# Optimization experiments

Measured on AMD Instinct MI355X. Metric: run time of the kernel, lower is better.

## Reference

```python
import jax, jax.numpy as jnp
import numpy as np

N = 64    # state dim n
K = 8     # mixture components
H = 1024  # fhat hidden
B = 65536
LOG2PI = float(np.log(2.0 * np.pi))

def setup_inputs() -> dict:
    key = jax.random.key(0)
    ks = jax.random.split(key, 8)
    x = jax.random.normal(ks[0], (B, N), jnp.float32)
    y = jax.random.normal(ks[1], (B, 1, N), jnp.float32)
    W1 = jax.random.normal(ks[2], (N, H), jnp.float32) / np.sqrt(N)
    b1 = jnp.zeros((H,), jnp.float32)
    W2 = jax.random.normal(ks[3], (H, 2 * K * N), jnp.float32) / np.sqrt(H)
    b2 = jnp.zeros((2 * K * N,), jnp.float32)
    Wp1 = jax.random.normal(ks[4], (N, N), jnp.float32) / np.sqrt(N)
    bp1 = jnp.zeros((N,), jnp.float32)
    Wp2 = jax.random.normal(ks[5], (N, K), jnp.float32) / np.sqrt(N)
    bp2 = jnp.zeros((K,), jnp.float32)
    return {"x": x, "y": y, "W1": W1, "b1": b1, "W2": W2, "b2": b2,
            "Wp1": Wp1, "bp1": bp1, "Wp2": Wp2, "bp2": bp2}

def _mdn_view(t):
    # torch.stack(t.split(n, dim=1)).view(-1, k, n): raw reshape of [k,B,n] -> [B,k,n]
    return jnp.stack(jnp.split(t, K, axis=1)).reshape(-1, K, N)

def reference(x, y, W1, b1, W2, b2, Wp1, bp1, Wp2, bp2):
    # fhat: Linear -> ELU -> Linear
    fhatx = jax.nn.elu(x @ W1 + b1) @ W2 + b2          # [B, 2*K*N]
    mu_raw, var_raw = jnp.split(fhatx, 2, axis=-1)     # each [B, K*N]
    mu = _mdn_view(mu_raw)                             # [B, K, N]
    var = jnp.maximum(jnp.exp(_mdn_view(var_raw)), 1e-8)
    # pi network: log probs of OneHotCategorical
    logits = jax.nn.elu(x @ Wp1 + bp1) @ Wp2 + bp2     # [B, K]
    log_pi = jax.nn.log_softmax(logits, axis=-1)
    # diagonal-covariance MVN log_prob (closed form, O(n))
    d = y - mu                                         # [B, K, N]
    logp_y = -0.5 * (jnp.sum(d * d / var + jnp.log(var), axis=-1) + N * LOG2PI)
    loss = jax.scipy.special.logsumexp(log_pi + logp_y, axis=-1)  # [B]
    return -jnp.mean(loss)
```

## Files before the change

kernel.cpp:

```cpp
#include <hip/hip_runtime.h>
#include <math.h>

typedef __attribute__((ext_vector_type(8))) _Float16 half8;
typedef __attribute__((ext_vector_type(4))) _Float16 half4;
typedef __attribute__((ext_vector_type(4))) float f32x4;

#define B_TOT 65536
#define LOG2PI_F 1.8378770664093453f
#define HALF_N_LOG2PI (0.5f * 64.0f * LOG2PI_F)
#define LOG_1EM8 (-18.420680743952367f)

#define WS_W2S  0
#define WS_W1P  (2u*1024*1024)
#define WS_LPS  (4u*1024*1024)
#define WS_PART (6u*1024*1024)
#define WS_HP   (8u*1024*1024)

typedef __attribute__((address_space(3))) unsigned int lds_u32;
typedef const __attribute__((address_space(1))) unsigned int glb_u32;

__device__ __forceinline__ void gload16(const void* g, void* l) {
    __builtin_amdgcn_global_load_lds((glb_u32*)g, (lds_u32*)l, 16, 0, 0);
}

__device__ __forceinline__ float eluf(float v) {
    return v > 0.0f ? v : __expf(v) - 1.0f;
}

__global__ __launch_bounds__(256)
void pack_w1(const float* __restrict__ src, _Float16* __restrict__ dst)
{
    __shared__ float ts[64][65];
    const int t = threadIdx.x;
    const int n0 = blockIdx.y * 64;
    {
        int r = t >> 2, c4 = t & 3;
        for (int i = 0; i < 4; ++i) {
            int cc = i * 4 + c4;
            float4 v = *(const float4*)&src[(size_t)r * 1024 + n0 + cc * 4];
            ts[r][cc*4+0] = v.x; ts[r][cc*4+1] = v.y;
            ts[r][cc*4+2] = v.z; ts[r][cc*4+3] = v.w;
        }
    }
    __syncthreads();
    {
        int n = t >> 2;
        for (int i = 0; i < 4; ++i) {
            int k = (i * 4 + (t & 3)) * 4;
            half4 h;
            h.x = (_Float16)ts[k+0][n];
            h.y = (_Float16)ts[k+1][n];
            h.z = (_Float16)ts[k+2][n];
            h.w = (_Float16)ts[k+3][n];
            size_t off = (size_t)(k >> 5) * 32768 + (size_t)(n0 + n) * 32 + (k & 31);
            *(half4*)&dst[off] = h;
        }
    }
}

__global__ __launch_bounds__(256)
void pack_w2s(const float* __restrict__ src, _Float16* __restrict__ dst)
{
    __shared__ float ts[64][65];
    const int t = threadIdx.x;
    const int k0 = blockIdx.x * 64, n0 = blockIdx.y * 64;
    {
        int r = t >> 2, c4 = t & 3;
        for (int i = 0; i < 4; ++i) {
            int cc = i * 4 + c4;
            float4 v = *(const float4*)&src[(size_t)(k0 + r) * 1024 + n0 + cc * 4];
            ts[r][cc*4+0] = v.x; ts[r][cc*4+1] = v.y;
            ts[r][cc*4+2] = v.z; ts[r][cc*4+3] = v.w;
        }
    }
    __syncthreads();
    {
        int n = t >> 2;
        int ng = n0 + n;
        for (int i = 0; i < 4; ++i) {
            int kl = (i * 4 + (t & 3)) * 4;
            int k = k0 + kl;
            half4 h;
            h.x = (_Float16)ts[kl+0][n];
            h.y = (_Float16)ts[kl+1][n];
            h.z = (_Float16)ts[kl+2][n];
            h.w = (_Float16)ts[kl+3][n];
            int kk = k & 31;
            int slot = ((kk >> 3) ^ ((ng >> 1) & 3));
            size_t off = (size_t)(k >> 5) * 32768 + (size_t)ng * 32 + (slot << 3) + (kk & 7);
            *(half4*)&dst[off] = h;
        }
    }
}

__global__ __launch_bounds__(512)
void k1_h(const float* __restrict__ x, const _Float16* __restrict__ W1P,
          const float* __restrict__ b1, _Float16* __restrict__ hp)
{
    __shared__ __align__(16) _Float16 xs[32 * 64];
    __shared__ __align__(16) _Float16 stage[32768];
    const int t = threadIdx.x, q = blockIdx.x;
    const int w = t >> 6, l = t & 63, g = l >> 4, l15 = l & 15;

    {
        const float4* x4 = (const float4*)x;
        int r = t >> 4, c = t & 15;
        float4 v = x4[(size_t)(q * 32 + r) * 16 + c];
        float vv[4] = {v.x, v.y, v.z, v.w};
        #pragma unroll
        for (int i = 0; i < 4; ++i) {
            int col = c * 4 + i;
            xs[r * 64 + (col ^ ((r & 7) << 3))] = (_Float16)vv[i];
        }
    }
    __syncthreads();

    f32x4 acc[8][2];
    const float4* b1_4 = (const float4*)b1;
    #pragma unroll
    for (int nf = 0; nf < 8; ++nf) {
        float4 bv = b1_4[(w * 128 + nf * 16 + 4 * g) >> 2];
        acc[nf][0] = (f32x4){bv.x, bv.y, bv.z, bv.w};
        acc[nf][1] = acc[nf][0];
    }
    #pragma unroll
    for (int k0 = 0; k0 < 64; k0 += 32) {
        half8 bx[2];
        #pragma unroll
        for (int rf = 0; rf < 2; ++rf) {
            int row = rf * 16 + l15;
            bx[rf] = *(const half8*)&xs[row * 64 + ((k0 + 8 * g) ^ ((row & 7) << 3))];
        }
        #pragma unroll
        for (int nf = 0; nf < 8; ++nf) {
            size_t off = (size_t)(k0 >> 5) * 32768 + (size_t)(w * 128 + nf * 16 + l15) * 32 + 8 * g;
            half8 aw = *(const half8*)&W1P[off];
            #pragma unroll
            for (int rf = 0; rf < 2; ++rf)
                acc[nf][rf] = __builtin_amdgcn_mfma_f32_16x16x32_f16(aw, bx[rf], acc[nf][rf], 0, 0, 0);
        }
    }
    #pragma unroll
    for (int nf = 0; nf < 8; ++nf) {
        int kt = w * 4 + (nf >> 1);
        int kkhi = (nf & 1) * 2 + (g >> 1);
        int kklo = 4 * (g & 1);
        #pragma unroll
        for (int rf = 0; rf < 2; ++rf) {
            int row = rf * 16 + l15;
            int slot = kkhi ^ ((row >> 1) & 3);
            half4 h4;
            h4.x = (_Float16)eluf(acc[nf][rf][0]);
            h4.y = (_Float16)eluf(acc[nf][rf][1]);
            h4.z = (_Float16)eluf(acc[nf][rf][2]);
            h4.w = (_Float16)eluf(acc[nf][rf][3]);
            *(half4*)&stage[kt * 1024 + row * 32 + slot * 8 + kklo] = h4;
        }
    }
    __syncthreads();
    #pragma unroll
    for (int i = 0; i < 8; ++i) {
        int f8 = (i * 512 + t) * 8;
        int kt = f8 >> 10;
        int rem = f8 & 1023;
        *(half8*)&hp[(size_t)kt * 2097152 + (size_t)q * 1024 + rem] = *(const half8*)&stage[f8];
    }
}

__global__ __launch_bounds__(512)
void k2_gemm2(const _Float16* __restrict__ hp, const _Float16* __restrict__ W2S,
              const float* __restrict__ b2, const float* __restrict__ y,
              float* __restrict__ lps)
{
    __shared__ __align__(16) _Float16 Ab[2][4096];
    __shared__ __align__(16) _Float16 Bb[2][8192];
    __shared__ float lpp[128][2][2];

    const int t = threadIdx.x;
    const int bid = blockIdx.x;
    const int logical = (bid & 7) * 256 + (bid >> 3);
    const int RT = logical >> 2;
    const int j  = logical & 3;
    const int w = t >> 6, l = t & 63, g = l >> 4, l15 = l & 15;
    const int wr = w >> 2, wc = w & 3;

    int bn[4];
    bn[0] = (wc >> 1) * 64 + (wc & 1) * 32 + l15;
    bn[1] = bn[0] + 16;
    bn[2] = bn[0] + 128;
    bn[3] = bn[1] + 128;

    f32x4 acc[4][4];
    #pragma unroll
    for (int fc = 0; fc < 4; ++fc) {
        int colg = (fc < 2) ? (j * 128 + bn[fc]) : (512 + j * 128 + bn[fc] - 128);
        float bv = b2[colg];
        #pragma unroll
        for (int fr = 0; fr < 4; ++fr) acc[fr][fc] = (f32x4){bv, bv, bv, bv};
    }

    const char* hpb  = (const char*)hp;
    const char* w2sb = (const char*)W2S;
    const int lane16 = l * 16;

    {
        size_t ga = ((size_t)0 * 65536 + (size_t)RT * 128) * 64 + w * 1024 + lane16;
        gload16(hpb + ga, (char*)&Ab[0][0] + w * 1024);
        size_t gb0 = ((size_t)0 * 1024 + j * 128) * 64 + w * 1024 + lane16;
        gload16(w2sb + gb0, (char*)&Bb[0][0] + w * 1024);
        size_t gb1 = ((size_t)0 * 1024 + 512 + j * 128) * 64 + w * 1024 + lane16;
        gload16(w2sb + gb1, (char*)&Bb[0][0] + 8192 + w * 1024);
    }
    __syncthreads();

    for (int kt = 0; kt < 32; ++kt) {
        int cur = kt & 1;
        if (kt < 31) {
            int nx = cur ^ 1;
            size_t ga = ((size_t)(kt + 1) * 65536 + (size_t)RT * 128) * 64 + w * 1024 + lane16;
            gload16(hpb + ga, (char*)&Ab[nx][0] + w * 1024);
            size_t gb0 = ((size_t)(kt + 1) * 1024 + j * 128) * 64 + w * 1024 + lane16;
            gload16(w2sb + gb0, (char*)&Bb[nx][0] + w * 1024);
            size_t gb1 = ((size_t)(kt + 1) * 1024 + 512 + j * 128) * 64 + w * 1024 + lane16;
            gload16(w2sb + gb1, (char*)&Bb[nx][0] + 8192 + w * 1024);
        }
        half8 aF[4], bF[4];
        #pragma unroll
        for (int fr = 0; fr < 4; ++fr) {
            int r = wr * 64 + fr * 16 + l15;
            aF[fr] = *(const half8*)((const char*)&Ab[cur][0] + r * 64 + ((g ^ ((r >> 1) & 3)) << 4));
        }
        #pragma unroll
        for (int fc = 0; fc < 4; ++fc) {
            int n = bn[fc];
            bF[fc] = *(const half8*)((const char*)&Bb[cur][0] + n * 64 + ((g ^ ((n >> 1) & 3)) << 4));
        }
        #pragma unroll
        for (int fc = 0; fc < 4; ++fc)
            #pragma unroll
            for (int fr = 0; fr < 4; ++fr)
                acc[fr][fc] = __builtin_amdgcn_mfma_f32_16x16x32_f16(aF[fr], bF[fc], acc[fr][fc], 0, 0, 0);
        __syncthreads();
    }

    const int jj = j * 2 + (wc >> 1);
    float s[4][4];
    #pragma unroll
    for (int fr = 0; fr < 4; ++fr)
        #pragma unroll
        for (int rg = 0; rg < 4; ++rg) s[fr][rg] = 0.0f;

    #pragma unroll
    for (int fc = 0; fc < 2; ++fc) {
        int n = (wc & 1) * 32 + fc * 16 + l15;
        #pragma unroll
        for (int fr = 0; fr < 4; ++fr)
            #pragma unroll
            for (int rg = 0; rg < 4; ++rg) {
                int grow = RT * 128 + wr * 64 + fr * 16 + 4 * g + rg;
                int bp = (grow >> 3) + jj * 8192;
                float yv = y[(size_t)bp * 64 + n];
                float mu = acc[fr][fc][rg];
                float vr = acc[fr][fc + 2][rg];
                float vre = fmaxf(vr, LOG_1EM8);
                float iv = (vr >= LOG_1EM8) ? expf(-vr) : 1e8f;
                float d = yv - mu;
                s[fr][rg] += fmaf(d * d, iv, vre);
            }
    }
    #pragma unroll
    for (int fr = 0; fr < 4; ++fr)
        #pragma unroll
        for (int rg = 0; rg < 4; ++rg) {
            float v = s[fr][rg];
            v += __shfl_xor(v, 1); v += __shfl_xor(v, 2);
            v += __shfl_xor(v, 4); v += __shfl_xor(v, 8);
            s[fr][rg] = v;
        }
    if (l15 == 0) {
        #pragma unroll
        for (int fr = 0; fr < 4; ++fr)
            #pragma unroll
            for (int rg = 0; rg < 4; ++rg)
                lpp[wr * 64 + fr * 16 + 4 * g + rg][wc >> 1][wc & 1] = s[fr][rg];
    }
    __syncthreads();
    if (t < 256) {
        int row_l = t >> 1, m = t & 1;
        float lp = -0.5f * (lpp[row_l][m][0] + lpp[row_l][m][1]) - HALF_N_LOG2PI;
        int grow = RT * 128 + row_l;
        int bp = (grow >> 3) + (j * 2 + m) * 8192;
        lps[(size_t)bp * 8 + (grow & 7)] = lp;
    }
}

__global__ __launch_bounds__(256)
void k3_pi(const float* __restrict__ x, const float* __restrict__ Wp1,
           const float* __restrict__ bp1, const float* __restrict__ Wp2,
           const float* __restrict__ bp2, const float* __restrict__ lps,
           float* __restrict__ partials)
{
    __shared__ float xsl[256][65];
    __shared__ float w1s[64][65];
    __shared__ float w2s[64][8];
    __shared__ float wsum[4];
    const int t = threadIdx.x;
    const int b0 = blockIdx.x * 256;

    {
        const float4* x4 = (const float4*)x;
        for (int i = 0; i < 16; ++i) {
            int idx = t + i * 256;
            int r = idx >> 4, c = idx & 15;
            float4 v = x4[(size_t)(b0 + r) * 16 + c];
            xsl[r][c*4+0] = v.x; xsl[r][c*4+1] = v.y;
            xsl[r][c*4+2] = v.z; xsl[r][c*4+3] = v.w;
        }
        for (int i = 0; i < 16; ++i) {
            int idx = t + i * 256;
            int r = idx >> 6, c = idx & 63;
            w1s[r][c] = Wp1[r * 64 + c];
        }
        ((float*)w2s)[t] = Wp2[t];
        ((float*)w2s)[t + 256] = Wp2[t + 256];
    }
    __syncthreads();

    float hid[64];
    #pragma unroll
    for (int c = 0; c < 64; ++c) hid[c] = bp1[c];
    for (int n = 0; n < 64; ++n) {
        float xv = xsl[t][n];
        #pragma unroll
        for (int c = 0; c < 64; ++c) hid[c] = fmaf(xv, w1s[n][c], hid[c]);
    }
    float lg[8];
    #pragma unroll
    for (int k = 0; k < 8; ++k) lg[k] = bp2[k];
    #pragma unroll
    for (int c = 0; c < 64; ++c) {
        float e = eluf(hid[c]);
        #pragma unroll
        for (int k = 0; k < 8; ++k) lg[k] = fmaf(e, w2s[c][k], lg[k]);
    }
    float4 lpa = *(const float4*)&lps[(size_t)(b0 + t) * 8];
    float4 lpb = *(const float4*)&lps[(size_t)(b0 + t) * 8 + 4];
    float lp[8] = {lpa.x, lpa.y, lpa.z, lpa.w, lpb.x, lpb.y, lpb.z, lpb.w};

    float m1 = lg[0];
    #pragma unroll
    for (int k = 1; k < 8; ++k) m1 = fmaxf(m1, lg[k]);
    float den = 0.0f;
    #pragma unroll
    for (int k = 0; k < 8; ++k) den += expf(lg[k] - m1);
    float lden = logf(den);

    float v0 = lg[0] - m1 - lden + lp[0];
    float m2 = v0;
    float vv[8]; vv[0] = v0;
    #pragma unroll
    for (int k = 1; k < 8; ++k) {
        vv[k] = lg[k] - m1 - lden + lp[k];
        m2 = fmaxf(m2, vv[k]);
    }
    float s2 = 0.0f;
    #pragma unroll
    for (int k = 0; k < 8; ++k) s2 += expf(vv[k] - m2);
    float loss = m2 + logf(s2);

    float ssum = loss;
    ssum += __shfl_xor(ssum, 1);  ssum += __shfl_xor(ssum, 2);
    ssum += __shfl_xor(ssum, 4);  ssum += __shfl_xor(ssum, 8);
    ssum += __shfl_xor(ssum, 16); ssum += __shfl_xor(ssum, 32);
    if ((t & 63) == 0) wsum[t >> 6] = ssum;
    __syncthreads();
    if (t == 0) partials[blockIdx.x] = wsum[0] + wsum[1] + wsum[2] + wsum[3];
}

__global__ void k4_reduce(const float* __restrict__ partials, float* __restrict__ out)
{
    __shared__ double red[256];
    int t = threadIdx.x;
    red[t] = (double)partials[t];
    __syncthreads();
    for (int s = 128; s > 0; s >>= 1) {
        if (t < s) red[t] += red[t + s];
        __syncthreads();
    }
    if (t == 0) out[0] = (float)(-red[0] / (double)B_TOT);
}

extern "C" void kernel_launch(void* const* d_in, const int* in_sizes, int n_in,
                              void* d_out, int out_size, void* d_ws, size_t ws_size,
                              hipStream_t stream)
{
    const float* x   = (const float*)d_in[0];
    const float* y   = (const float*)d_in[1];
    const float* W1  = (const float*)d_in[2];
    const float* b1  = (const float*)d_in[3];
    const float* W2  = (const float*)d_in[4];
    const float* b2  = (const float*)d_in[5];
    const float* Wp1 = (const float*)d_in[6];
    const float* bp1 = (const float*)d_in[7];
    const float* Wp2 = (const float*)d_in[8];
    const float* bp2 = (const float*)d_in[9];

    char* ws = (char*)d_ws;
    _Float16* W2S = (_Float16*)(ws + WS_W2S);
    _Float16* W1P = (_Float16*)(ws + WS_W1P);
    float* lps      = (float*)(ws + WS_LPS);
    float* partials = (float*)(ws + WS_PART);
    _Float16* hp    = (_Float16*)(ws + WS_HP);

    pack_w2s<<<dim3(16, 16), 256, 0, stream>>>(W2, W2S);
    pack_w1<<<dim3(1, 16), 256, 0, stream>>>(W1, W1P);
    k1_h<<<2048, 512, 0, stream>>>(x, W1P, b1, hp);
    k2_gemm2<<<2048, 512, 0, stream>>>(hp, W2S, b2, y, lps);
    k3_pi<<<256, 256, 0, stream>>>(x, Wp1, bp1, Wp2, bp2, lps, partials);
    k4_reduce<<<1, 256, 0, stream>>>(partials, (float*)d_out);
}
```

Measured before the change: 225.0 us.

## Enlarge GEMM2 tile to 256x256 with K=64 steps and phased LDS pipeline

The second GEMM kernel now uses a 256-row by 256-column block tile with 64-deep K stages in a 130KB LDS buffer. It halves the grid and interleaves global-to-LDS prefetch with MFMA sub-phases under fine-grained barriers. The epilogue is restructured: variance-holding waves compute exp(-var) into LDS, and mean-holding waves then combine it with y to form the log-probs. This is meant to raise arithmetic intensity and cut global traffic per FLOP, at the cost of one block per CU occupancy and many barriers.

```diff
diff --git a/kernel.cpp b/kernel.cpp
--- a/kernel.cpp
+++ b/kernel.cpp
@@ -172,125 +172,173 @@
               const float* __restrict__ b2, const float* __restrict__ y,
               float* __restrict__ lps)
 {
-    __shared__ __align__(16) _Float16 Ab[2][4096];
-    __shared__ __align__(16) _Float16 Bb[2][8192];
-    __shared__ float lpp[128][2][2];
+    __shared__ __align__(16) char smem[133120];
+    float* vrs = (float*)(smem + 131072);
 
     const int t = threadIdx.x;
     const int bid = blockIdx.x;
-    const int logical = (bid & 7) * 256 + (bid >> 3);
+    const int logical = (bid & 7) * 128 + (bid >> 3);
     const int RT = logical >> 2;
     const int j  = logical & 3;
     const int w = t >> 6, l = t & 63, g = l >> 4, l15 = l & 15;
     const int wr = w >> 2, wc = w & 3;
 
-    int bn[4];
-    bn[0] = (wc >> 1) * 64 + (wc & 1) * 32 + l15;
-    bn[1] = bn[0] + 16;
-    bn[2] = bn[0] + 128;
-    bn[3] = bn[1] + 128;
-
-    f32x4 acc[4][4];
-    #pragma unroll
-    for (int fc = 0; fc < 4; ++fc) {
-        int colg = (fc < 2) ? (j * 128 + bn[fc]) : (512 + j * 128 + bn[fc] - 128);
+    f32x4 acc[8][4];
+    #pragma unroll
+    for (int C = 0; C < 4; ++C) {
+        int colg = (wc < 2) ? (j * 128 + wc * 64 + C * 16 + l15)
+                            : (512 + j * 128 + (wc - 2) * 64 + C * 16 + l15);
         float bv = b2[colg];
         #pragma unroll
-        for (int fr = 0; fr < 4; ++fr) acc[fr][fc] = (f32x4){bv, bv, bv, bv};
-    }
-
-    const char* hpb  = (const char*)hp;
-    const char* w2sb = (const char*)W2S;
-    const int lane16 = l * 16;
-
-    {
-        size_t ga = ((size_t)0 * 65536 + (size_t)RT * 128) * 64 + w * 1024 + lane16;
-        gload16(hpb + ga, (char*)&Ab[0][0] + w * 1024);
-        size_t gb0 = ((size_t)0 * 1024 + j * 128) * 64 + w * 1024 + lane16;
-        gload16(w2sb + gb0, (char*)&Bb[0][0] + w * 1024);
-        size_t gb1 = ((size_t)0 * 1024 + 512 + j * 128) * 64 + w * 1024 + lane16;
-        gload16(w2sb + gb1, (char*)&Bb[0][0] + 8192 + w * 1024);
-    }
-    __syncthreads();
-
-    for (int kt = 0; kt < 32; ++kt) {
-        int cur = kt & 1;
-        if (kt < 31) {
-            int nx = cur ^ 1;
-            size_t ga = ((size_t)(kt + 1) * 65536 + (size_t)RT * 128) * 64 + w * 1024 + lane16;
-            gload16(hpb + ga, (char*)&Ab[nx][0] + w * 1024);
-            size_t gb0 = ((size_t)(kt + 1) * 1024 + j * 128) * 64 + w * 1024 + lane16;
-            gload16(w2sb + gb0, (char*)&Bb[nx][0] + w * 1024);
-            size_t gb1 = ((size_t)(kt + 1) * 1024 + 512 + j * 128) * 64 + w * 1024 + lane16;
-            gload16(w2sb + gb1, (char*)&Bb[nx][0] + 8192 + w * 1024);
-        }
-        half8 aF[4], bF[4];
-        #pragma unroll
-        for (int fr = 0; fr < 4; ++fr) {
-            int r = wr * 64 + fr * 16 + l15;
-            aF[fr] = *(const half8*)((const char*)&Ab[cur][0] + r * 64 + ((g ^ ((r >> 1) & 3)) << 4));
-        }
-        #pragma unroll
-        for (int fc = 0; fc < 4; ++fc) {
-            int n = bn[fc];
-            bF[fc] = *(const half8*)((const char*)&Bb[cur][0] + n * 64 + ((g ^ ((n >> 1) & 3)) << 4));
-        }
-        #pragma unroll
-        for (int fc = 0; fc < 4; ++fc)
-            #pragma unroll
-            for (int fr = 0; fr < 4; ++fr)
-                acc[fr][fc] = __builtin_amdgcn_mfma_f32_16x16x32_f16(aF[fr], bF[fc], acc[fr][fc], 0, 0, 0);
-        __syncthreads();
-    }
-
-    const int jj = j * 2 + (wc >> 1);
-    float s[4][4];
-    #pragma unroll
-    for (int fr = 0; fr < 4; ++fr)
-        #pragma unroll
-        for (int rg = 0; rg < 4; ++rg) s[fr][rg] = 0.0f;
-
-    #pragma unroll
-    for (int fc = 0; fc < 2; ++fc) {
-        int n = (wc & 1) * 32 + fc * 16 + l15;
-        #pragma unroll
-        for (int fr = 0; fr < 4; ++fr)
+        for (int R = 0; R < 8; ++R) acc[R][C] = (f32x4){bv, bv, bv, bv};
+    }
+
+    const char* hpA = (const char*)hp  + (size_t)RT * 16384;
+    const char* w2B = (const char*)W2S + (size_t)j * 8192;
+    const int voff = w * 1024 + l * 16;
+    const int wl   = w * 1024;
+
+    #define GLA(KT,B,KH,PART)                                                          \
+        gload16(hpA + (size_t)(2*(KT)+(KH)) * 4194304 + (PART)*8192 + voff,            \
+                smem + (B)*32768 + (KH)*16384 + (PART)*8192 + wl)
+    #define GLB(KT,B,KH,HALF)                                                          \
+        gload16(w2B + (size_t)(2*(KT)+(KH)) * 65536 + (HALF)*32768 + voff,             \
+                smem + 65536 + (B)*32768 + (KH)*16384 + (HALF)*8192 + wl)
+
+    half8 aF[4][2], bF0[2][2], bF1[2][2];
+
+    #define RDA(CUR,RH) {                                                              \
+        _Pragma("unroll") for (int rf = 0; rf < 4; ++rf) {                             \
+            int r = wr*128 + (RH)*64 + rf*16 + l15;                                    \
+            int sw = (g ^ ((r >> 1) & 3)) << 4;                                        \
+            aF[rf][0] = *(const half8*)(smem + (CUR)*32768 + r*64 + sw);               \
+            aF[rf][1] = *(const half8*)(smem + (CUR)*32768 + 16384 + r*64 + sw); } }
+    #define RDB(CUR,CH,DST) {                                                          \
+        _Pragma("unroll") for (int fc = 0; fc < 2; ++fc) {                             \
+            int n2 = (wc & 1)*64 + (CH)*32 + fc*16 + l15;                              \
+            int sw = (g ^ ((n2 >> 1) & 3)) << 4;                                       \
+            int hb = 65536 + (CUR)*32768 + (wc >> 1)*8192 + n2*64 + sw;                \
+            DST[fc][0] = *(const half8*)(smem + hb);                                   \
+            DST[fc][1] = *(const half8*)(smem + hb + 16384); } }
+    #define MF(RH,CH,BF) {                                                             \
+        _Pragma("unroll") for (int ks = 0; ks < 2; ++ks)                               \
+        _Pragma("unroll") for (int fc = 0; fc < 2; ++fc)                               \
+        _Pragma("unroll") for (int rf = 0; rf < 4; ++rf)                               \
+            acc[(RH)*4+rf][(CH)*2+fc] = __builtin_amdgcn_mfma_f32_16x16x32_f16(        \
+                aF[rf][ks], BF[fc][ks], acc[(RH)*4+rf][(CH)*2+fc], 0, 0, 0); }
+
+    #define KT_BODY(KT,CUR,NXT,PRE) {                                                  \
+        asm volatile("s_waitcnt vmcnt(0)" ::: "memory");                               \
+        __builtin_amdgcn_s_barrier();                                                  \
+        RDA(CUR,0); RDB(CUR,0,bF0);                                                    \
+        if (PRE) { GLA((KT)+1,NXT,0,0); GLA((KT)+1,NXT,0,1); }                         \
+        __builtin_amdgcn_s_barrier();                                                  \
+        MF(0,0,bF0);                                                                   \
+        __builtin_amdgcn_s_barrier();                                                  \
+        RDB(CUR,1,bF1);                                                                \
+        if (PRE) { GLA((KT)+1,NXT,1,0); GLA((KT)+1,NXT,1,1); }                         \
+        __builtin_amdgcn_s_barrier();                                                  \
+        MF(0,1,bF1);                                                                   \
+        __builtin_amdgcn_s_barrier();                                                  \
+        RDA(CUR,1);                                                                    \
+        if (PRE) { GLB((KT)+1,NXT,0,0); GLB((KT)+1,NXT,0,1); }                         \
+        __builtin_amdgcn_s_barrier();                                                  \
+        MF(1,0,bF0);                                                                   \
+        __builtin_amdgcn_s_barrier();                                                  \
+        if (PRE) { GLB((KT)+1,NXT,1,0); GLB((KT)+1,NXT,1,1); }                         \
+        __builtin_amdgcn_s_barrier();                                                  \
+        MF(1,1,bF1);                                                                   \
+        __builtin_amdgcn_s_barrier(); }
+
+    GLA(0,0,0,0); GLA(0,0,0,1); GLA(0,0,1,0); GLA(0,0,1,1);
+    GLB(0,0,0,0); GLB(0,0,0,1); GLB(0,0,1,0); GLB(0,0,1,1);
+
+    #pragma unroll 1
+    for (int kt2 = 0; kt2 < 8; ++kt2) {
+        const int kt = kt2 * 2;
+        KT_BODY(kt,     0, 1, (kt     < 15));
+        KT_BODY(kt + 1, 1, 0, (kt + 1 < 15));
+    }
+    #undef KT_BODY
+    #undef MF
+    #undef RDB
+    #undef RDA
+    #undef GLB
+    #undef GLA
+
+    __syncthreads();
+    float* ivr = (float*)smem;
+    const int region = wr * 2 + (wc & 1);
+
+    if (wc >= 2) {
+        float rs[8][4];
+        #pragma unroll
+        for (int R = 0; R < 8; ++R)
+            #pragma unroll
+            for (int rg = 0; rg < 4; ++rg) rs[R][rg] = 0.0f;
+        #pragma unroll
+        for (int R = 0; R < 8; ++R)
+            #pragma unroll
+            for (int C = 0; C < 4; ++C)
+                #pragma unroll
+                for (int rg = 0; rg < 4; ++rg) {
+                    float vr = acc[R][C][rg];
+                    float vre = fmaxf(vr, LOG_1EM8);
+                    float iv = (vr >= LOG_1EM8) ? expf(-vr) : 1e8f;
+                    rs[R][rg] += vre;
+                    int rowL = R * 16 + 4 * g + rg;
+                    int colL = C * 16 + l15;
+                    ivr[region * 8192 + rowL * 64 + (colL ^ (((rowL >> 2) & 1) << 4))] = iv;
+                }
+        #pragma unroll
+        for (int R = 0; R < 8; ++R)
             #pragma unroll
             for (int rg = 0; rg < 4; ++rg) {
-                int grow = RT * 128 + wr * 64 + fr * 16 + 4 * g + rg;
-                int bp = (grow >> 3) + jj * 8192;
-                float yv = y[(size_t)bp * 64 + n];
-                float mu = acc[fr][fc][rg];
-                float vr = acc[fr][fc + 2][rg];
-                float vre = fmaxf(vr, LOG_1EM8);
-                float iv = (vr >= LOG_1EM8) ? expf(-vr) : 1e8f;
-                float d = yv - mu;
-                s[fr][rg] += fmaf(d * d, iv, vre);
+                float v = rs[R][rg];
+                v += __shfl_xor(v, 1); v += __shfl_xor(v, 2);
+                v += __shfl_xor(v, 4); v += __shfl_xor(v, 8);
+                if (l15 == 0)
+                    vrs[(wr * 128 + R * 16 + 4 * g + rg) * 2 + (wc & 1)] = v;
             }
     }
-    #pragma unroll
-    for (int fr = 0; fr < 4; ++fr)
-        #pragma unroll
-        for (int rg = 0; rg < 4; ++rg) {
-            float v = s[fr][rg];
-            v += __shfl_xor(v, 1); v += __shfl_xor(v, 2);
-            v += __shfl_xor(v, 4); v += __shfl_xor(v, 8);
-            s[fr][rg] = v;
-        }
-    if (l15 == 0) {
-        #pragma unroll
-        for (int fr = 0; fr < 4; ++fr)
-            #pragma unroll
-            for (int rg = 0; rg < 4; ++rg)
-                lpp[wr * 64 + fr * 16 + 4 * g + rg][wc >> 1][wc & 1] = s[fr][rg];
-    }
-    __syncthreads();
-    if (t < 256) {
-        int row_l = t >> 1, m = t & 1;
-        float lp = -0.5f * (lpp[row_l][m][0] + lpp[row_l][m][1]) - HALF_N_LOG2PI;
-        int grow = RT * 128 + row_l;
-        int bp = (grow >> 3) + (j * 2 + m) * 8192;
-        lps[(size_t)bp * 8 + (grow & 7)] = lp;
+    __syncthreads();
+
+    if (wc < 2) {
+        const int m = 2 * j + wc;
+        float rs[8][4];
+        #pragma unroll
+        for (int R = 0; R < 8; ++R)
+            #pragma unroll
+            for (int rg = 0; rg < 4; ++rg) rs[R][rg] = 0.0f;
+        #pragma unroll
+        for (int R = 0; R < 8; ++R)
+            #pragma unroll
+            for (int C = 0; C < 4; ++C)
+                #pragma unroll
+                for (int rg = 0; rg < 4; ++rg) {
+                    int rowL = R * 16 + 4 * g + rg;
+                    int grow = RT * 256 + wr * 128 + rowL;
+                    int bp = (grow >> 3) + m * 8192;
+                    float yv = y[(size_t)bp * 64 + C * 16 + l15];
+                    float iv = ivr[region * 8192 + rowL * 64 + ((C * 16 + l15) ^ (((rowL >> 2) & 1) << 4))];
+                    float d = yv - acc[R][C][rg];
+                    rs[R][rg] = fmaf(d * d, iv, rs[R][rg]);
+                }
+        #pragma unroll
+        for (int R = 0; R < 8; ++R)
+            #pragma unroll
+            for (int rg = 0; rg < 4; ++rg) {
+                float v = rs[R][rg];
+                v += __shfl_xor(v, 1); v += __shfl_xor(v, 2);
+                v += __shfl_xor(v, 4); v += __shfl_xor(v, 8);
+                if (l15 == 0) {
+                    int rowL = R * 16 + 4 * g + rg;
+                    int grow = RT * 256 + wr * 128 + rowL;
+                    float lp = -0.5f * (v + vrs[(wr * 128 + rowL) * 2 + wc]) - HALF_N_LOG2PI;
+                    int bp = (grow >> 3) + m * 8192;
+                    lps[(size_t)bp * 8 + (grow & 7)] = lp;
+                }
+            }
     }
 }
 
@@ -415,7 +463,7 @@
     pack_w2s<<<dim3(16, 16), 256, 0, stream>>>(W2, W2S);
     pack_w1<<<dim3(1, 16), 256, 0, stream>>>(W1, W1P);
     k1_h<<<2048, 512, 0, stream>>>(x, W1P, b1, hp);
-    k2_gemm2<<<2048, 512, 0, stream>>>(hp, W2S, b2, y, lps);
+    k2_gemm2<<<1024, 512, 0, stream>>>(hp, W2S, b2, y, lps);
     k3_pi<<<256, 256, 0, stream>>>(x, Wp1, bp1, Wp2, bp2, lps, partials);
     k4_reduce<<<1, 256, 0, stream>>>(partials, (float*)d_out);
 }
```

New measurement: 308.4 us. 37.0% more time.
